# Optimization experiments

Measured on AMD Instinct MI355X. Metric: run time of the kernel, lower is better.

## Reference

```python
import jax, jax.numpy as jnp
import numpy as np

B, C_FEATS, T = 8, 256, 1024
NUM_COMP = 64
EPS = 1e-9


def setup_inputs() -> dict:
    key = jax.random.key(0)
    k1, k2 = jax.random.split(key)
    x = jax.random.normal(k1, (B, C_FEATS, T), dtype=jnp.float32)
    mu = jax.random.normal(k2, (NUM_COMP, C_FEATS), dtype=jnp.float32)
    prec = jnp.ones((NUM_COMP,), dtype=jnp.float32)
    return {"x": x, "mu": mu, "prec": prec}


def reference(x, mu, prec):
    # x: (B, F, T) -> (B, T, F), matching torch transpose(1, -1)
    xt = jnp.swapaxes(x, 1, 2)
    # squared distance to each centroid via expansion (avoids (B,T,C,F) delta):
    x2 = jnp.sum(xt * xt, axis=-1, keepdims=True)            # (B, T, 1)
    mu2 = jnp.sum(mu * mu, axis=-1)                           # (C,)
    xmu = jnp.einsum('btf,cf->btc', xt, mu)                   # (B, T, C)
    dist = x2 - 2.0 * xmu + mu2                               # (B, T, C)
    llk = -(prec * prec) * dist                               # use_bias=False
    r = jax.nn.softmax(llk, axis=-1)                          # (B, T, C)
    Nraw = jnp.sum(r, axis=1)                                 # (B, C)
    N = Nraw + EPS
    # F = sum_t r*(x - mu) = sum_t r*x - (sum_t r)*mu
    F = jnp.einsum('btc,btf->bcf', r, xt) - Nraw[..., None] * mu  # (B, C, F)
    pool = F / N[..., None]
    return pool.reshape(x.shape[0], -1)                       # (B, C*F)
```

## Files before the change

kernel.cpp:

```cpp
#include <hip/hip_runtime.h>

#define BB 8
#define FF 256
#define TT 1024
#define CC 64
#define TCHUNK 16
#define NTILE 64
#define NBLK (BB * NTILE)
constexpr float EPS = 1e-9f;

#define WS_MU2   0
#define WS_P2    64
#define WS_NPART 128
#define WS_FPART 32896

__global__ __launch_bounds__(256) void prep_kernel(const float* __restrict__ mu,
                                                   const float* __restrict__ prec,
                                                   float* __restrict__ ws) {
    const int tid = threadIdx.x;
    const int c = tid >> 2, q = tid & 3;
    const float* mp = mu + c * FF + q * 64;
    float s = 0.f;
    #pragma unroll
    for (int i = 0; i < 16; ++i) {
        float4 v = *(const float4*)(mp + i * 4);
        s += v.x * v.x + v.y * v.y + v.z * v.z + v.w * v.w;
    }
    s += __shfl_xor(s, 1);
    s += __shfl_xor(s, 2);
    if (q == 0) ws[WS_MU2 + c] = s;
    if (tid < CC) { float p = prec[tid]; ws[WS_P2 + tid] = p * p; }
}

#define XS_STRIDE 260
#define SR_STRIDE 68
#define RL_STRIDE 68

__global__ __launch_bounds__(256) void fused_kernel(const float* __restrict__ x,
                                                    const float* __restrict__ mu,
                                                    float* __restrict__ ws) {
    __shared__ __align__(16) float xt[TCHUNK][XS_STRIDE];
    __shared__ __align__(16) float Sred[4][TCHUNK][SR_STRIDE];
    __shared__ __align__(16) float rl[TCHUNK][RL_STRIDE];
    __shared__ float x2s[TCHUNK];
    __shared__ float mu2s[CC], p2s[CC];

    const int tid = threadIdx.x;
    const int b    = blockIdx.x >> 6;
    const int tile = blockIdx.x & 63;
    const int t0   = tile * TCHUNK;
    const float* xb = x + (size_t)b * FF * TT;

    #pragma unroll
    for (int i = 0; i < 4; ++i) {
        const int id = i * 256 + tid;
        const int f = id >> 2, seg = id & 3;
        float4 v = *(const float4*)(xb + f * TT + t0 + seg * 4);
        xt[seg * 4 + 0][f] = v.x;
        xt[seg * 4 + 1][f] = v.y;
        xt[seg * 4 + 2][f] = v.z;
        xt[seg * 4 + 3][f] = v.w;
    }
    if (tid < CC) { mu2s[tid] = ws[WS_MU2 + tid]; p2s[tid] = ws[WS_P2 + tid]; }
    __syncthreads();

    {
        const int t = tid >> 4, kk = tid & 15;
        float s = 0.f;
        #pragma unroll
        for (int q = 0; q < 16; ++q) { float v = xt[t][kk + 16 * q]; s += v * v; }
        s += __shfl_xor(s, 1);
        s += __shfl_xor(s, 2);
        s += __shfl_xor(s, 4);
        s += __shfl_xor(s, 8);
        if (kk == 0) x2s[t] = s;
    }
    __syncthreads();

    {
        const int g = tid >> 6;
        const int lane = tid & 63;
        const int tr = lane & 7;
        const int tcc = lane >> 3;
        const int c0 = tcc * 8;
        float acc[2][8];
        #pragma unroll
        for (int i = 0; i < 2; ++i)
            #pragma unroll
            for (int j = 0; j < 8; ++j) acc[i][j] = 0.f;

        const float* mupt = mu + (size_t)c0 * FF + g * 64;
        #pragma unroll 4
        for (int kk = 0; kk < 16; ++kk) {
            const int f4 = g * 64 + kk * 4;
            float4 xv0 = *(const float4*)&xt[tr][f4];
            float4 xv1 = *(const float4*)&xt[tr + 8][f4];
            #pragma unroll
            for (int j = 0; j < 8; ++j) {
                float4 mv = *(const float4*)(mupt + j * FF + kk * 4);
                acc[0][j] += xv0.x * mv.x + xv0.y * mv.y + xv0.z * mv.z + xv0.w * mv.w;
                acc[1][j] += xv1.x * mv.x + xv1.y * mv.y + xv1.z * mv.z + xv1.w * mv.w;
            }
        }
        #pragma unroll
        for (int i = 0; i < 2; ++i) {
            *(float4*)&Sred[g][tr + 8 * i][c0] =
                make_float4(acc[i][0], acc[i][1], acc[i][2], acc[i][3]);
            *(float4*)&Sred[g][tr + 8 * i][c0 + 4] =
                make_float4(acc[i][4], acc[i][5], acc[i][6], acc[i][7]);
        }
    }
    __syncthreads();

    {
        const int t = tid >> 4, kk = tid & 15;
        const int c4 = kk * 4;
        float Sx = 0.f, Sy = 0.f, Sz = 0.f, Sw = 0.f;
        #pragma unroll
        for (int gg = 0; gg < 4; ++gg) {
            float4 v = *(const float4*)&Sred[gg][t][c4];
            Sx += v.x; Sy += v.y; Sz += v.z; Sw += v.w;
        }
        const float x2v = x2s[t];
        float l0 = -p2s[c4 + 0] * (x2v - 2.f * Sx + mu2s[c4 + 0]);
        float l1 = -p2s[c4 + 1] * (x2v - 2.f * Sy + mu2s[c4 + 1]);
        float l2 = -p2s[c4 + 2] * (x2v - 2.f * Sz + mu2s[c4 + 2]);
        float l3 = -p2s[c4 + 3] * (x2v - 2.f * Sw + mu2s[c4 + 3]);
        float m = fmaxf(fmaxf(l0, l1), fmaxf(l2, l3));
        m = fmaxf(m, __shfl_xor(m, 1));
        m = fmaxf(m, __shfl_xor(m, 2));
        m = fmaxf(m, __shfl_xor(m, 4));
        m = fmaxf(m, __shfl_xor(m, 8));
        float e0 = __expf(l0 - m), e1 = __expf(l1 - m);
        float e2 = __expf(l2 - m), e3 = __expf(l3 - m);
        float sum = e0 + e1 + e2 + e3;
        sum += __shfl_xor(sum, 1);
        sum += __shfl_xor(sum, 2);
        sum += __shfl_xor(sum, 4);
        sum += __shfl_xor(sum, 8);
        const float inv = 1.f / sum;
        *(float4*)&rl[t][c4] = make_float4(e0 * inv, e1 * inv, e2 * inv, e3 * inv);
    }
    __syncthreads();

    if (tid < CC) {
        float ns = 0.f;
        #pragma unroll
        for (int t = 0; t < TCHUNK; ++t) ns += rl[t][tid];
        ws[WS_NPART + (size_t)blockIdx.x * CC + tid] = ns;
    }

    {
        const int fc = tid & 15;
        const int cc = tid >> 4;
        const int c0 = cc * 4;
        float a2[4][4][4];
        #pragma unroll
        for (int j = 0; j < 4; ++j)
            #pragma unroll
            for (int q = 0; q < 4; ++q)
                #pragma unroll
                for (int e = 0; e < 4; ++e) a2[j][q][e] = 0.f;

        #pragma unroll 4
        for (int t = 0; t < TCHUNK; ++t) {
            float4 rv = *(const float4*)&rl[t][c0];
            #pragma unroll
            for (int q = 0; q < 4; ++q) {
                float4 xv = *(const float4*)&xt[t][fc * 4 + 64 * q];
                a2[0][q][0] += rv.x * xv.x; a2[0][q][1] += rv.x * xv.y;
                a2[0][q][2] += rv.x * xv.z; a2[0][q][3] += rv.x * xv.w;
                a2[1][q][0] += rv.y * xv.x; a2[1][q][1] += rv.y * xv.y;
                a2[1][q][2] += rv.y * xv.z; a2[1][q][3] += rv.y * xv.w;
                a2[2][q][0] += rv.z * xv.x; a2[2][q][1] += rv.z * xv.y;
                a2[2][q][2] += rv.z * xv.z; a2[2][q][3] += rv.z * xv.w;
                a2[3][q][0] += rv.w * xv.x; a2[3][q][1] += rv.w * xv.y;
                a2[3][q][2] += rv.w * xv.z; a2[3][q][3] += rv.w * xv.w;
            }
        }
        float* fp = ws + WS_FPART + (size_t)blockIdx.x * CC * FF;
        #pragma unroll
        for (int j = 0; j < 4; ++j)
            #pragma unroll
            for (int q = 0; q < 4; ++q)
                *(float4*)(fp + (c0 + j) * FF + fc * 4 + 64 * q) =
                    make_float4(a2[j][q][0], a2[j][q][1], a2[j][q][2], a2[j][q][3]);
    }
}

__global__ __launch_bounds__(256) void final_kernel(const float* __restrict__ mu,
                                                    const float* __restrict__ ws,
                                                    float* __restrict__ out) {
    const int bid = blockIdx.x;
    const int b = bid >> 6, c = bid & 63;
    const int f = threadIdx.x;
    const float* fp = ws + WS_FPART + (size_t)(b * NTILE) * CC * FF + c * FF + f;
    float s = 0.f;
    #pragma unroll 8
    for (int tile = 0; tile < NTILE; ++tile) s += fp[(size_t)tile * CC * FF];
    const float* np = ws + WS_NPART + (size_t)(b * NTILE) * CC + c;
    float nr = 0.f;
    #pragma unroll 8
    for (int tile = 0; tile < NTILE; ++tile) nr += np[tile * CC];
    const float mv = mu[c * FF + f];
    out[((size_t)b * CC + c) * FF + f] = (s - nr * mv) / (nr + EPS);
}

extern "C" void kernel_launch(void* const* d_in, const int* in_sizes, int n_in,
                              void* d_out, int out_size, void* d_ws, size_t ws_size,
                              hipStream_t stream) {
    const float* x    = (const float*)d_in[0];
    const float* mu   = (const float*)d_in[1];
    const float* prec = (const float*)d_in[2];
    float* out = (float*)d_out;
    float* ws  = (float*)d_ws;

    prep_kernel<<<1, 256, 0, stream>>>(mu, prec, ws);
    fused_kernel<<<NBLK, 256, 0, stream>>>(x, mu, ws);
    final_kernel<<<NBLK, 256, 0, stream>>>(mu, ws, out);
}
```

Before: 41.07 us.

## Split F accumulation into separate pass over stored responsibilities with larger time tiles

Pass A now computes and stores the softmax responsibilities r to the workspace instead of F partials over 16-step chunks. A new pass B re-reads x and r in 64-step time tiles to build F partials, so there are only 16 partials per batch. This cuts the workspace write and final-reduction traffic, in exchange for re-reading x and an extra r round trip. It also folds the mu² and prec² prep into pass A, so each block recomputes them and one launch is removed.

Measured after the change: 33.44 us. -18.6%, faster.

```diff
diff --git a/kernel.cpp b/kernel.cpp
--- a/kernel.cpp
+++ b/kernel.cpp
@@ -4,44 +4,25 @@
 #define FF 256
 #define TT 1024
 #define CC 64
+constexpr float EPS = 1e-9f;
+
 #define TCHUNK 16
 #define NTILE 64
-#define NBLK (BB * NTILE)
-constexpr float EPS = 1e-9f;
-
-#define WS_MU2   0
-#define WS_P2    64
-#define WS_NPART 128
-#define WS_FPART 32896
-
-__global__ __launch_bounds__(256) void prep_kernel(const float* __restrict__ mu,
-                                                   const float* __restrict__ prec,
-                                                   float* __restrict__ ws) {
-    const int tid = threadIdx.x;
-    const int c = tid >> 2, q = tid & 3;
-    const float* mp = mu + c * FF + q * 64;
-    float s = 0.f;
-    #pragma unroll
-    for (int i = 0; i < 16; ++i) {
-        float4 v = *(const float4*)(mp + i * 4);
-        s += v.x * v.x + v.y * v.y + v.z * v.z + v.w * v.w;
-    }
-    s += __shfl_xor(s, 1);
-    s += __shfl_xor(s, 2);
-    if (q == 0) ws[WS_MU2 + c] = s;
-    if (tid < CC) { float p = prec[tid]; ws[WS_P2 + tid] = p * p; }
-}
-
-#define XS_STRIDE 260
-#define SR_STRIDE 68
-#define RL_STRIDE 68
-
-__global__ __launch_bounds__(256) void fused_kernel(const float* __restrict__ x,
+#define BT 64
+#define NTQ 16
+#define BCF (BB * CC * FF)
+
+#define WS_R   0
+#define WS_NP  524288
+#define WS_FP  557056
+
+__global__ __launch_bounds__(256) void passA_kernel(const float* __restrict__ x,
                                                     const float* __restrict__ mu,
+                                                    const float* __restrict__ prec,
                                                     float* __restrict__ ws) {
-    __shared__ __align__(16) float xt[TCHUNK][XS_STRIDE];
-    __shared__ __align__(16) float Sred[4][TCHUNK][SR_STRIDE];
-    __shared__ __align__(16) float rl[TCHUNK][RL_STRIDE];
+    __shared__ __align__(16) float xt[TCHUNK][260];
+    __shared__ __align__(16) float Sred[4][TCHUNK][68];
+    __shared__ __align__(16) float rl[TCHUNK][68];
     __shared__ float x2s[TCHUNK];
     __shared__ float mu2s[CC], p2s[CC];
 
@@ -50,6 +31,21 @@
     const int tile = blockIdx.x & 63;
     const int t0   = tile * TCHUNK;
     const float* xb = x + (size_t)b * FF * TT;
+
+    {
+        const int c = tid >> 2, q = tid & 3;
+        const float* mp = mu + c * FF + q * 64;
+        float s = 0.f;
+        #pragma unroll
+        for (int i = 0; i < 16; ++i) {
+            float4 v = *(const float4*)(mp + i * 4);
+            s += v.x * v.x + v.y * v.y + v.z * v.z + v.w * v.w;
+        }
+        s += __shfl_xor(s, 1);
+        s += __shfl_xor(s, 2);
+        if (q == 0) mu2s[c] = s;
+        if (tid < CC) { float p = prec[tid]; p2s[tid] = p * p; }
+    }
 
     #pragma unroll
     for (int i = 0; i < 4; ++i) {
@@ -61,7 +57,6 @@
         xt[seg * 4 + 2][f] = v.z;
         xt[seg * 4 + 3][f] = v.w;
     }
-    if (tid < CC) { mu2s[tid] = ws[WS_MU2 + tid]; p2s[tid] = ws[WS_P2 + tid]; }
     __syncthreads();
 
     {
@@ -81,8 +76,7 @@
         const int g = tid >> 6;
         const int lane = tid & 63;
         const int tr = lane & 7;
-        const int tcc = lane >> 3;
-        const int c0 = tcc * 8;
+        const int c0 = (lane >> 3) * 8;
         float acc[2][8];
         #pragma unroll
         for (int i = 0; i < 2; ++i)
@@ -147,63 +141,94 @@
         float ns = 0.f;
         #pragma unroll
         for (int t = 0; t < TCHUNK; ++t) ns += rl[t][tid];
-        ws[WS_NPART + (size_t)blockIdx.x * CC + tid] = ns;
-    }
-
-    {
-        const int fc = tid & 15;
-        const int cc = tid >> 4;
-        const int c0 = cc * 4;
-        float a2[4][4][4];
-        #pragma unroll
-        for (int j = 0; j < 4; ++j)
-            #pragma unroll
-            for (int q = 0; q < 4; ++q)
-                #pragma unroll
-                for (int e = 0; e < 4; ++e) a2[j][q][e] = 0.f;
-
-        #pragma unroll 4
-        for (int t = 0; t < TCHUNK; ++t) {
-            float4 rv = *(const float4*)&rl[t][c0];
-            #pragma unroll
-            for (int q = 0; q < 4; ++q) {
-                float4 xv = *(const float4*)&xt[t][fc * 4 + 64 * q];
-                a2[0][q][0] += rv.x * xv.x; a2[0][q][1] += rv.x * xv.y;
-                a2[0][q][2] += rv.x * xv.z; a2[0][q][3] += rv.x * xv.w;
-                a2[1][q][0] += rv.y * xv.x; a2[1][q][1] += rv.y * xv.y;
-                a2[1][q][2] += rv.y * xv.z; a2[1][q][3] += rv.y * xv.w;
-                a2[2][q][0] += rv.z * xv.x; a2[2][q][1] += rv.z * xv.y;
-                a2[2][q][2] += rv.z * xv.z; a2[2][q][3] += rv.z * xv.w;
-                a2[3][q][0] += rv.w * xv.x; a2[3][q][1] += rv.w * xv.y;
-                a2[3][q][2] += rv.w * xv.z; a2[3][q][3] += rv.w * xv.w;
-            }
-        }
-        float* fp = ws + WS_FPART + (size_t)blockIdx.x * CC * FF;
-        #pragma unroll
-        for (int j = 0; j < 4; ++j)
-            #pragma unroll
-            for (int q = 0; q < 4; ++q)
-                *(float4*)(fp + (c0 + j) * FF + fc * 4 + 64 * q) =
-                    make_float4(a2[j][q][0], a2[j][q][1], a2[j][q][2], a2[j][q][3]);
-    }
+        ws[WS_NP + (size_t)blockIdx.x * CC + tid] = ns;
+    }
+
+    {
+        const int c = tid >> 2, seg = tid & 3;
+        float4 v;
+        v.x = rl[seg * 4 + 0][c];
+        v.y = rl[seg * 4 + 1][c];
+        v.z = rl[seg * 4 + 2][c];
+        v.w = rl[seg * 4 + 3][c];
+        *(float4*)(ws + WS_R + ((size_t)b * CC + c) * TT + t0 + seg * 4) = v;
+    }
+}
+
+__global__ __launch_bounds__(256) void passB_kernel(const float* __restrict__ x,
+                                                    float* __restrict__ ws) {
+    __shared__ __align__(16) float xs[BT][68];
+    __shared__ __align__(16) float rs[CC][68];
+    const int tid = threadIdx.x;
+    const int bid = blockIdx.x;
+    const int b   = bid >> 6;
+    const int fsl = (bid >> 4) & 3;
+    const int tq  = bid & 15;
+    const int f0  = fsl * 64;
+    const int t0  = tq * BT;
+    const float* xb = x + (size_t)b * FF * TT;
+    const float* rb = ws + WS_R + (size_t)b * CC * TT;
+
+    #pragma unroll
+    for (int it = 0; it < 4; ++it) {
+        const int id = it * 256 + tid;
+        {
+            const int ff = id >> 4, seg = id & 15;
+            float4 v = *(const float4*)(xb + (f0 + ff) * TT + t0 + seg * 4);
+            xs[seg * 4 + 0][ff] = v.x;
+            xs[seg * 4 + 1][ff] = v.y;
+            xs[seg * 4 + 2][ff] = v.z;
+            xs[seg * 4 + 3][ff] = v.w;
+        }
+        {
+            const int c = id >> 4, cs = id & 15;
+            float4 v = *(const float4*)(rb + (size_t)c * TT + t0 + cs * 4);
+            *(float4*)&rs[c][cs * 4] = v;
+        }
+    }
+    __syncthreads();
+
+    const int fi = tid & 15, cg = tid >> 4;
+    float acc[4][4];
+    #pragma unroll
+    for (int j = 0; j < 4; ++j)
+        #pragma unroll
+        for (int e = 0; e < 4; ++e) acc[j][e] = 0.f;
+
+    #pragma unroll 8
+    for (int t = 0; t < BT; ++t) {
+        float4 xv = *(const float4*)&xs[t][fi * 4];
+        #pragma unroll
+        for (int j = 0; j < 4; ++j) {
+            float rv = rs[cg * 4 + j][t];
+            acc[j][0] += rv * xv.x;
+            acc[j][1] += rv * xv.y;
+            acc[j][2] += rv * xv.z;
+            acc[j][3] += rv * xv.w;
+        }
+    }
+
+    float* fp = ws + WS_FP + (size_t)tq * BCF + (size_t)b * CC * FF;
+    #pragma unroll
+    for (int j = 0; j < 4; ++j)
+        *(float4*)(fp + (cg * 4 + j) * FF + f0 + fi * 4) =
+            make_float4(acc[j][0], acc[j][1], acc[j][2], acc[j][3]);
 }
 
 __global__ __launch_bounds__(256) void final_kernel(const float* __restrict__ mu,
                                                     const float* __restrict__ ws,
                                                     float* __restrict__ out) {
-    const int bid = blockIdx.x;
-    const int b = bid >> 6, c = bid & 63;
+    const int b = blockIdx.x >> 6, c = blockIdx.x & 63;
     const int f = threadIdx.x;
-    const float* fp = ws + WS_FPART + (size_t)(b * NTILE) * CC * FF + c * FF + f;
+    float nr = 0.f;
+    const float* np = ws + WS_NP + (size_t)b * NTILE * CC + c;
+    #pragma unroll
+    for (int tile = 0; tile < NTILE; ++tile) nr += np[tile * CC];
+    const float* fp = ws + WS_FP + (size_t)b * CC * FF + c * FF + f;
     float s = 0.f;
-    #pragma unroll 8
-    for (int tile = 0; tile < NTILE; ++tile) s += fp[(size_t)tile * CC * FF];
-    const float* np = ws + WS_NPART + (size_t)(b * NTILE) * CC + c;
-    float nr = 0.f;
-    #pragma unroll 8
-    for (int tile = 0; tile < NTILE; ++tile) nr += np[tile * CC];
-    const float mv = mu[c * FF + f];
-    out[((size_t)b * CC + c) * FF + f] = (s - nr * mv) / (nr + EPS);
+    #pragma unroll
+    for (int p = 0; p < NTQ; ++p) s += fp[(size_t)p * BCF];
+    out[((size_t)b * CC + c) * FF + f] = (s - nr * mu[c * FF + f]) / (nr + EPS);
 }
 
 extern "C" void kernel_launch(void* const* d_in, const int* in_sizes, int n_in,
@@ -215,7 +240,7 @@
     float* out = (float*)d_out;
     float* ws  = (float*)d_ws;
 
-    prep_kernel<<<1, 256, 0, stream>>>(mu, prec, ws);
-    fused_kernel<<<NBLK, 256, 0, stream>>>(x, mu, ws);
-    final_kernel<<<NBLK, 256, 0, stream>>>(mu, ws, out);
-}
+    passA_kernel<<<512, 256, 0, stream>>>(x, mu, prec, ws);
+    passB_kernel<<<512, 256, 0, stream>>>(x, ws);
+    final_kernel<<<512, 256, 0, stream>>>(mu, ws, out);
+}
```
